# Optimization experiments

Measured on AMD Instinct MI355X. Metric: run time of the kernel, lower is better.

The kernel has to match this reference:

```python
import jax, jax.numpy as jnp
import numpy as np

VOCAB = 50257
EMB = 512
HID = 1024
H = HID // 2  # per-direction hidden
TAGS = 24
START = 22
STOP = 23
SEQ = 4096
NEG = -10000.0


def setup_inputs() -> dict:
    key = jax.random.key(0)
    ks = jax.random.split(key, 16)
    s = 1.0 / np.sqrt(H)
    u = lambda k, shp: jax.random.uniform(k, shp, jnp.float32, -s, s)
    sentence = jax.random.randint(ks[0], (SEQ,), 0, VOCAB)
    emb = jax.random.normal(ks[1], (VOCAB, EMB), jnp.float32)
    w_ih_f = u(ks[2], (4 * H, EMB)); w_hh_f = u(ks[3], (4 * H, H))
    b_ih_f = u(ks[4], (4 * H,));    b_hh_f = u(ks[5], (4 * H,))
    w_ih_b = u(ks[6], (4 * H, EMB)); w_hh_b = u(ks[7], (4 * H, H))
    b_ih_b = u(ks[8], (4 * H,));    b_hh_b = u(ks[9], (4 * H,))
    w_tag = u(ks[10], (TAGS, HID)); b_tag = u(ks[11], (TAGS,))
    transitions = jax.random.normal(ks[12], (TAGS, TAGS), jnp.float32)
    transitions = transitions.at[START, :].set(NEG).at[:, STOP].set(NEG)
    h0 = jax.random.normal(ks[13], (2, H), jnp.float32)  # [dir, H]
    c0 = jax.random.normal(ks[14], (2, H), jnp.float32)
    return dict(sentence=sentence, emb=emb,
                w_ih_f=w_ih_f, w_hh_f=w_hh_f, b_ih_f=b_ih_f, b_hh_f=b_hh_f,
                w_ih_b=w_ih_b, w_hh_b=w_hh_b, b_ih_b=b_ih_b, b_hh_b=b_hh_b,
                w_tag=w_tag, b_tag=b_tag, transitions=transitions, h0=h0, c0=c0)


def _lstm_dir(x, w_ih, w_hh, b_ih, b_hh, h, c, reverse):
    # x: [T, EMB]; precompute input projections once
    xg = x @ w_ih.T + (b_ih + b_hh)  # [T, 4H]
    def step(carry, xt):
        h, c = carry
        g = xt + h @ w_hh.T
        i, f, gg, o = jnp.split(g, 4)
        i = jax.nn.sigmoid(i); f = jax.nn.sigmoid(f)
        gg = jnp.tanh(gg);     o = jax.nn.sigmoid(o)
        c = f * c + i * gg
        h = o * jnp.tanh(c)
        return (h, c), h
    _, hs = jax.lax.scan(step, (h, c), xg, reverse=reverse)
    return hs  # [T, H]


def reference(sentence, emb, w_ih_f, w_hh_f, b_ih_f, b_hh_f,
              w_ih_b, w_hh_b, b_ih_b, b_hh_b, w_tag, b_tag,
              transitions, h0, c0):
    x = emb[sentence]  # [T, EMB]
    hf = _lstm_dir(x, w_ih_f, w_hh_f, b_ih_f, b_hh_f, h0[0], c0[0], False)
    hb = _lstm_dir(x, w_ih_b, w_hh_b, b_ih_b, b_hh_b, h0[1], c0[1], True)
    lstm_out = jnp.concatenate([hf, hb], axis=-1)          # [T, HID]
    feats = lstm_out @ w_tag.T + b_tag                     # [T, TAGS]

    # Viterbi: max-plus recursion over tags, vectorized per timestep
    fv0 = jnp.full((TAGS,), NEG, jnp.float32).at[START].set(0.0)
    def vstep(fv, feat):
        scores = transitions + fv[None, :]                 # [next, prev]
        bp = jnp.argmax(scores, axis=1)
        return jnp.max(scores, axis=1) + feat, bp
    fv, bps = jax.lax.scan(vstep, fv0, feats)              # bps: [T, TAGS]

    terminal = fv + transitions[STOP]
    best = jnp.argmax(terminal)
    path_score = terminal[best]

    def btstep(tag, bp):
        prev = bp[tag]
        return prev, prev
    _, ys = jax.lax.scan(btstep, best, bps, reverse=True)  # ys[t] = tag at t-1; ys[0]==START
    best_path = jnp.concatenate([ys[1:], best[None]]).astype(jnp.int32)
    return path_score, best_path
```

## Files before the change

kernel.cpp:

```cpp
#include <hip/hip_runtime.h>
#include <cstdint>
#include <cstddef>

#define T_SEQ 4096
#define EMB_D 512
#define HDIM 512
#define G4 2048
#define NTAGS 24
#define START_TAG 22
#define STOP_TAG 23
#define NEGV -10000.0f
#define NBLK 32
#define HSLICE 16
#define SENT 0xFFFFFFFFu

__global__ __launch_bounds__(256) void gemm_xg_kernel(
    const int* __restrict__ sent, const float* __restrict__ emb,
    const float* __restrict__ w_ih_f, const float* __restrict__ b_ih_f, const float* __restrict__ b_hh_f,
    const float* __restrict__ w_ih_b, const float* __restrict__ b_ih_b, const float* __restrict__ b_hh_b,
    float* __restrict__ xg)
{
    const int dir = blockIdx.z;
    const float* W  = dir ? w_ih_b : w_ih_f;
    const float* bi = dir ? b_ih_b : b_ih_f;
    const float* bh = dir ? b_hh_b : b_hh_f;
    const int m0 = blockIdx.y * 64;
    const int n0 = blockIdx.x * 64;
    const int tid = threadIdx.x;

    __shared__ __attribute__((aligned(16))) float As[32][64];
    __shared__ __attribute__((aligned(16))) float Bs[32][64];

    const int lrow = tid >> 2;
    const int lk   = (tid & 3) * 8;

    const int srow = sent[m0 + lrow];
    const float* aptr = emb + (size_t)srow * EMB_D + lk;
    const float* bptr = W   + (size_t)(n0 + lrow) * EMB_D + lk;

    const int ty = tid >> 4;
    const int tx = tid & 15;

    float acc[4][4];
    #pragma unroll
    for (int i = 0; i < 4; ++i)
        #pragma unroll
        for (int j = 0; j < 4; ++j) acc[i][j] = 0.f;

    for (int kk = 0; kk < EMB_D; kk += 32) {
        float4 a0 = *(const float4*)(aptr + kk);
        float4 a1 = *(const float4*)(aptr + kk + 4);
        float4 b0 = *(const float4*)(bptr + kk);
        float4 b1 = *(const float4*)(bptr + kk + 4);
        __syncthreads();
        As[lk+0][lrow]=a0.x; As[lk+1][lrow]=a0.y; As[lk+2][lrow]=a0.z; As[lk+3][lrow]=a0.w;
        As[lk+4][lrow]=a1.x; As[lk+5][lrow]=a1.y; As[lk+6][lrow]=a1.z; As[lk+7][lrow]=a1.w;
        Bs[lk+0][lrow]=b0.x; Bs[lk+1][lrow]=b0.y; Bs[lk+2][lrow]=b0.z; Bs[lk+3][lrow]=b0.w;
        Bs[lk+4][lrow]=b1.x; Bs[lk+5][lrow]=b1.y; Bs[lk+6][lrow]=b1.z; Bs[lk+7][lrow]=b1.w;
        __syncthreads();
        #pragma unroll
        for (int k = 0; k < 32; ++k) {
            float4 av = *(const float4*)&As[k][ty*4];
            float4 bv = *(const float4*)&Bs[k][tx*4];
            acc[0][0]+=av.x*bv.x; acc[0][1]+=av.x*bv.y; acc[0][2]+=av.x*bv.z; acc[0][3]+=av.x*bv.w;
            acc[1][0]+=av.y*bv.x; acc[1][1]+=av.y*bv.y; acc[1][2]+=av.y*bv.z; acc[1][3]+=av.y*bv.w;
            acc[2][0]+=av.z*bv.x; acc[2][1]+=av.z*bv.y; acc[2][2]+=av.z*bv.z; acc[2][3]+=av.z*bv.w;
            acc[3][0]+=av.w*bv.x; acc[3][1]+=av.w*bv.y; acc[3][2]+=av.w*bv.z; acc[3][3]+=av.w*bv.w;
        }
    }
    #pragma unroll
    for (int i = 0; i < 4; ++i) {
        const int t = m0 + ty*4 + i;
        float* crow = xg + ((size_t)dir*T_SEQ + t) * G4 + n0 + tx*4;
        #pragma unroll
        for (int j = 0; j < 4; ++j) {
            const int jg = n0 + tx*4 + j;
            crow[j] = acc[i][j] + bi[jg] + bh[jg];
        }
    }
}

__global__ __attribute__((amdgpu_waves_per_eu(2, 2))) __launch_bounds__(512)
void bilstm_kernel(
    const float* __restrict__ w_hh_f, const float* __restrict__ w_hh_b,
    const float* __restrict__ h0, const float* __restrict__ c0,
    const float* __restrict__ xg,
    uint32_t* __restrict__ h_hist,
    int* __restrict__ claim)
{
    uint32_t xcc;
    asm volatile("s_getreg_b32 %0, hwreg(HW_REG_XCC_ID)" : "=s"(xcc));
    xcc &= 7u;

    __shared__ int rank_s;
    if (threadIdx.x == 0)
        rank_s = __hip_atomic_fetch_add(&claim[xcc], 1, __ATOMIC_RELAXED,
                                        __HIP_MEMORY_SCOPE_AGENT);
    __syncthreads();
    const int rank = rank_s;

    int dir;
    if (xcc == 0) dir = 0;
    else if (xcc == 1) dir = 1;
    else return;
    if (rank >= NBLK) return;
    const int b = rank;

    const int tid = threadIdx.x;
    const int q   = tid >> 6;
    const int rl  = tid & 63;
    const int g2  = rl >> 4;
    const int hu  = rl & 15;
    const int row = g2 * HDIM + b * HSLICE + hu;

    const float* Wrow = (dir ? w_hh_b : w_hh_f) + (size_t)row * HDIM + q * 64;
    float w[64];
    #pragma unroll
    for (int j = 0; j < 16; ++j) {
        float4 v = ((const float4*)Wrow)[j];
        w[4*j+0]=v.x; w[4*j+1]=v.y; w[4*j+2]=v.z; w[4*j+3]=v.w;
    }
    #pragma unroll
    for (int i = 0; i < 64; ++i) asm volatile("" : "+v"(w[i]));

    __shared__ __attribute__((aligned(16))) float part[2][512];

    float c = (tid < HSLICE) ? c0[dir*HDIM + b*HSLICE + tid] : 0.f;

    const float* xgd = xg + (size_t)dir * T_SEQ * G4;
    uint32_t* hh = h_hist + (size_t)dir * T_SEQ * HDIM;

    float xv_cur = 0.f;
    if (tid < 64) {
        const int t0 = dir ? (T_SEQ - 1) : 0;
        xv_cur = xgd[(size_t)t0 * G4 + row];
    }

    for (int idx = 0; idx < T_SEQ; ++idx) {
        const int t = dir ? (T_SEQ - 1 - idx) : idx;

        float xv_nxt = 0.f;
        if (tid < 64 && idx + 1 < T_SEQ) {
            const int tn = dir ? (t - 1) : (t + 1);
            xv_nxt = xgd[(size_t)tn * G4 + row];
        }

        float hv;
        if (idx == 0) {
            hv = h0[dir*HDIM + tid];
        } else {
            const int tprev = dir ? (t + 1) : (t - 1);
            const uint32_t* wp = hh + (size_t)tprev*HDIM + tid;
            uint32_t u;
            do {
                u = __hip_atomic_load(wp, __ATOMIC_RELAXED, __HIP_MEMORY_SCOPE_AGENT);
            } while (u == SENT);
            union { uint32_t uu; float f; } cv; cv.uu = u;
            hv = cv.f;
        }

        const uint32_t hvu = __float_as_uint(hv);
        float s = 0.f;
        #pragma unroll
        for (int j = 0; j < 16; ++j) {
            const float h0v = __uint_as_float((uint32_t)__builtin_amdgcn_readlane((int)hvu, 4*j+0));
            const float h1v = __uint_as_float((uint32_t)__builtin_amdgcn_readlane((int)hvu, 4*j+1));
            const float h2v = __uint_as_float((uint32_t)__builtin_amdgcn_readlane((int)hvu, 4*j+2));
            const float h3v = __uint_as_float((uint32_t)__builtin_amdgcn_readlane((int)hvu, 4*j+3));
            s += w[4*j+0]*h0v + w[4*j+1]*h1v + w[4*j+2]*h2v + w[4*j+3]*h3v;
        }
        part[idx & 1][tid] = s;
        __syncthreads();

        if (tid < 64) {
            float g = xv_cur;
            const float* pb = part[idx & 1];
            #pragma unroll
            for (int qq = 0; qq < 8; ++qq) g += pb[qq*64 + tid];
            g = (g2 == 2) ? tanhf(g) : 1.f/(1.f + expf(-g));
            float iv = __shfl(g, hu);
            float fg = __shfl(g, hu + 16);
            float gv = __shfl(g, hu + 32);
            float ov = __shfl(g, hu + 48);
            if (tid < HSLICE) {
                c = fg*c + iv*gv;
                union { float f; uint32_t u; } hb; hb.f = ov * tanhf(c);
                __hip_atomic_store(hh + (size_t)t*HDIM + b*HSLICE + tid, hb.u,
                                   __ATOMIC_RELAXED, __HIP_MEMORY_SCOPE_AGENT);
            }
        }
        xv_cur = xv_nxt;
    }
}

__global__ __launch_bounds__(256) void feats_kernel(
    const float* __restrict__ h_hist, const float* __restrict__ w_tag,
    const float* __restrict__ b_tag, float* __restrict__ feats)
{
    const int t = blockIdx.x;
    const int tid = threadIdx.x;
    __shared__ __attribute__((aligned(16))) float h[1024];
    __shared__ float partl[192];
    for (int i = tid; i < 512; i += 256) {
        h[i]     = h_hist[(size_t)t*HDIM + i];
        h[512+i] = h_hist[(size_t)T_SEQ*HDIM + (size_t)t*HDIM + i];
    }
    __syncthreads();
    if (tid < 192) {
        const int tag = tid >> 3, p = tid & 7;
        const float* wr = w_tag + (size_t)tag*1024 + p*128;
        const float* hp = h + p*128;
        float s = 0.f;
        #pragma unroll 8
        for (int j = 0; j < 128; ++j) s += wr[j]*hp[j];
        partl[tid] = s;
    }
    __syncthreads();
    if (tid < NTAGS) {
        float s = b_tag[tid];
        #pragma unroll
        for (int p = 0; p < 8; ++p) s += partl[tid*8+p];
        feats[(size_t)t*NTAGS + tid] = s;
    }
}

__global__ void viterbi_fwd_kernel(
    const float* __restrict__ feats, const float* __restrict__ trans,
    float* __restrict__ d_out, unsigned char* __restrict__ bp,
    int* __restrict__ best_tag)
{
    const int lane = threadIdx.x;
    const bool act = lane < NTAGS;
    float tr[NTAGS];
    #pragma unroll
    for (int p = 0; p < NTAGS; ++p)
        tr[p] = act ? trans[lane*NTAGS + p] : NEGV;

    float fv = (lane == START_TAG) ? 0.f : NEGV;
    __shared__ float fvs[NTAGS];
    __shared__ float term[NTAGS];

    float ftn = act ? feats[lane] : 0.f;
    for (int t = 0; t < T_SEQ; ++t) {
        if (act) fvs[lane] = fv;
        __syncthreads();
        float ft = ftn;
        if (act && t + 1 < T_SEQ) ftn = feats[(size_t)(t+1)*NTAGS + lane];
        float bestv = -3.4e38f;
        int argp = 0;
        #pragma unroll
        for (int p = 0; p < NTAGS; ++p) {
            float sc = tr[p] + fvs[p];
            if (sc > bestv) { bestv = sc; argp = p; }
        }
        __syncthreads();
        fv = bestv + ft;
        if (act) bp[(size_t)t*NTAGS + lane] = (unsigned char)argp;
    }
    if (act) { fv += trans[STOP_TAG*NTAGS + lane]; term[lane] = fv; }
    __syncthreads();
    if (lane == 0) {
        float bv = term[0]; int bi = 0;
        #pragma unroll
        for (int p = 1; p < NTAGS; ++p) if (term[p] > bv) { bv = term[p]; bi = p; }
        d_out[0] = bv;
        *best_tag = bi;
    }
}

__global__ void bt_compose_kernel(const unsigned char* __restrict__ bp,
                                  unsigned char* __restrict__ segmap)
{
    const int s = blockIdx.x;
    const int tid = threadIdx.x;
    __shared__ __attribute__((aligned(16))) unsigned char lbp[64*NTAGS];
    const uint32_t* src = (const uint32_t*)(bp + (size_t)s * 64 * NTAGS);
    uint32_t* dst = (uint32_t*)lbp;
    #pragma unroll
    for (int i = 0; i < 6; ++i) dst[tid + 64*i] = src[tid + 64*i];
    __syncthreads();
    if (tid < NTAGS) {
        int m = tid;
        for (int tt = 63; tt >= 0; --tt) m = lbp[tt*NTAGS + m];
        segmap[s*NTAGS + tid] = (unsigned char)m;
    }
}

__global__ void bt_final_kernel(const unsigned char* __restrict__ segmap,
                                const int* __restrict__ best_tag,
                                int* __restrict__ end_tags)
{
    if (threadIdx.x == 0) {
        int tag = *best_tag;
        end_tags[63] = tag;
        for (int s = 63; s >= 1; --s) {
            tag = segmap[s*NTAGS + tag];
            end_tags[s-1] = tag;
        }
    }
}

__global__ void bt_write_kernel(const unsigned char* __restrict__ bp,
                                const int* __restrict__ end_tags,
                                float* __restrict__ out_path)
{
    const int s = blockIdx.x;
    const int tid = threadIdx.x;
    __shared__ __attribute__((aligned(16))) unsigned char lbp[64*NTAGS];
    const uint32_t* src = (const uint32_t*)(bp + (size_t)s * 64 * NTAGS);
    uint32_t* dst = (uint32_t*)lbp;
    #pragma unroll
    for (int i = 0; i < 6; ++i) dst[tid + 64*i] = src[tid + 64*i];
    __syncthreads();
    if (tid == 0) {
        int tag = end_tags[s];
        out_path[s*64 + 63] = (float)tag;
        for (int tt = 63; tt >= 1; --tt) {
            tag = lbp[tt*NTAGS + tag];
            out_path[s*64 + tt - 1] = (float)tag;
        }
    }
}

extern "C" void kernel_launch(void* const* d_in, const int* in_sizes, int n_in,
                              void* d_out, int out_size, void* d_ws, size_t ws_size,
                              hipStream_t stream)
{
    const int*   sent   = (const int*)d_in[0];
    const float* emb    = (const float*)d_in[1];
    const float* w_ih_f = (const float*)d_in[2];
    const float* w_hh_f = (const float*)d_in[3];
    const float* b_ih_f = (const float*)d_in[4];
    const float* b_hh_f = (const float*)d_in[5];
    const float* w_ih_b = (const float*)d_in[6];
    const float* w_hh_b = (const float*)d_in[7];
    const float* b_ih_b = (const float*)d_in[8];
    const float* b_hh_b = (const float*)d_in[9];
    const float* w_tag  = (const float*)d_in[10];
    const float* b_tag  = (const float*)d_in[11];
    const float* trans  = (const float*)d_in[12];
    const float* h0     = (const float*)d_in[13];
    const float* c0     = (const float*)d_in[14];
    float* out = (float*)d_out;

    char* ws = (char*)d_ws;
    size_t off = 0;
    auto alloc = [&](size_t bytes) {
        char* p = ws + off; off += (bytes + 255) & ~(size_t)255; return p;
    };
    float* xg      = (float*)alloc((size_t)2*T_SEQ*G4*sizeof(float));
    uint32_t* h_hist = (uint32_t*)alloc((size_t)2*T_SEQ*HDIM*sizeof(float));
    float* feats   = (float*)alloc((size_t)T_SEQ*NTAGS*sizeof(float));
    unsigned char* bp     = (unsigned char*)alloc((size_t)T_SEQ*NTAGS);
    unsigned char* segmap = (unsigned char*)alloc(64*NTAGS);
    int* best_tag = (int*)alloc(sizeof(int));
    int* end_tags = (int*)alloc(64*sizeof(int));
    int* claim    = (int*)alloc(8*sizeof(int));

    if (off > ws_size) {
        hipMemsetAsync(d_out, 0xFF, 4, stream);
        return;
    }

    hipMemsetAsync(h_hist, 0xFF, (size_t)2*T_SEQ*HDIM*sizeof(float), stream);
    hipMemsetAsync(claim, 0, 8*sizeof(int), stream);

    dim3 gg(G4/64, T_SEQ/64, 2);
    gemm_xg_kernel<<<gg, 256, 0, stream>>>(sent, emb,
        w_ih_f, b_ih_f, b_hh_f, w_ih_b, b_ih_b, b_hh_b, xg);
    bilstm_kernel<<<512, 512, 0, stream>>>(w_hh_f, w_hh_b, h0, c0, xg, h_hist, claim);
    feats_kernel<<<T_SEQ, 256, 0, stream>>>((const float*)h_hist, w_tag, b_tag, feats);
    viterbi_fwd_kernel<<<1, 64, 0, stream>>>(feats, trans, out, bp, best_tag);
    bt_compose_kernel<<<64, 64, 0, stream>>>(bp, segmap);
    bt_final_kernel<<<1, 64, 0, stream>>>(segmap, best_tag, end_tags);
    bt_write_kernel<<<64, 64, 0, stream>>>(bp, end_tags, out + 1);
}
```

Before: 8.850 ms.

## Restructure LSTM recurrent step so each wave owns whole hidden units

Work in the recurrent kernel is redistributed. Each wave now computes all four gates for two hidden units, with eight lanes splitting the K dimension. The incoming h vector is staged in padded LDS and read as float4, replacing 64 readlanes per lane. Partial sums are reduced with intra-wave shuffles, which removes the cross-wave LDS reduction, its second barrier, and the serial activation tail that ran only in wave 0. The cost is extra shuffle work and an LDS round trip for h on every timestep.

```diff
diff --git a/kernel.cpp b/kernel.cpp
--- a/kernel.cpp
+++ b/kernel.cpp
@@ -108,12 +108,14 @@
 
     const int tid = threadIdx.x;
     const int q   = tid >> 6;
-    const int rl  = tid & 63;
-    const int g2  = rl >> 4;
-    const int hu  = rl & 15;
-    const int row = g2 * HDIM + b * HSLICE + hu;
-
-    const float* Wrow = (dir ? w_hh_b : w_hh_f) + (size_t)row * HDIM + q * 64;
+    const int l   = tid & 63;
+    const int r   = l >> 3;
+    const int i   = l & 7;
+    const int gate = r & 3;
+    const int huo  = r >> 2;
+    const int row  = gate * HDIM + b * HSLICE + 2*q + huo;
+
+    const float* Wrow = (dir ? w_hh_b : w_hh_f) + (size_t)row * HDIM + i * 64;
     float w[64];
     #pragma unroll
     for (int j = 0; j < 16; ++j) {
@@ -121,29 +123,27 @@
         w[4*j+0]=v.x; w[4*j+1]=v.y; w[4*j+2]=v.z; w[4*j+3]=v.w;
     }
     #pragma unroll
-    for (int i = 0; i < 64; ++i) asm volatile("" : "+v"(w[i]));
-
-    __shared__ __attribute__((aligned(16))) float part[2][512];
-
-    float c = (tid < HSLICE) ? c0[dir*HDIM + b*HSLICE + tid] : 0.f;
+    for (int ii = 0; ii < 64; ++ii) asm volatile("" : "+v"(w[ii]));
+
+    __shared__ __attribute__((aligned(16))) float hbuf[2][544];
+
+    float c = 0.f;
+    if (i == 0 && gate == 0)
+        c = c0[dir*HDIM + b*HSLICE + 2*q + huo];
 
     const float* xgd = xg + (size_t)dir * T_SEQ * G4;
     uint32_t* hh = h_hist + (size_t)dir * T_SEQ * HDIM;
+    const bool leader = (i == 0);
 
     float xv_cur = 0.f;
-    if (tid < 64) {
+    if (leader) {
         const int t0 = dir ? (T_SEQ - 1) : 0;
         xv_cur = xgd[(size_t)t0 * G4 + row];
     }
 
     for (int idx = 0; idx < T_SEQ; ++idx) {
         const int t = dir ? (T_SEQ - 1 - idx) : idx;
-
-        float xv_nxt = 0.f;
-        if (tid < 64 && idx + 1 < T_SEQ) {
-            const int tn = dir ? (t - 1) : (t + 1);
-            xv_nxt = xgd[(size_t)tn * G4 + row];
-        }
+        const int p = idx & 1;
 
         float hv;
         if (idx == 0) {
@@ -158,36 +158,44 @@
             union { uint32_t uu; float f; } cv; cv.uu = u;
             hv = cv.f;
         }
-
-        const uint32_t hvu = __float_as_uint(hv);
+        hbuf[p][q*68 + l] = hv;
+        __syncthreads();
+
+        float xv_nxt = 0.f;
+        if (leader && idx + 1 < T_SEQ) {
+            const int tn = dir ? (t - 1) : (t + 1);
+            xv_nxt = xgd[(size_t)tn * G4 + row];
+        }
+
+        const float4* hb4 = (const float4*)&hbuf[p][i*68];
         float s = 0.f;
         #pragma unroll
         for (int j = 0; j < 16; ++j) {
-            const float h0v = __uint_as_float((uint32_t)__builtin_amdgcn_readlane((int)hvu, 4*j+0));
-            const float h1v = __uint_as_float((uint32_t)__builtin_amdgcn_readlane((int)hvu, 4*j+1));
-            const float h2v = __uint_as_float((uint32_t)__builtin_amdgcn_readlane((int)hvu, 4*j+2));
-            const float h3v = __uint_as_float((uint32_t)__builtin_amdgcn_readlane((int)hvu, 4*j+3));
-            s += w[4*j+0]*h0v + w[4*j+1]*h1v + w[4*j+2]*h2v + w[4*j+3]*h3v;
-        }
-        part[idx & 1][tid] = s;
-        __syncthreads();
-
-        if (tid < 64) {
-            float g = xv_cur;
-            const float* pb = part[idx & 1];
-            #pragma unroll
-            for (int qq = 0; qq < 8; ++qq) g += pb[qq*64 + tid];
-            g = (g2 == 2) ? tanhf(g) : 1.f/(1.f + expf(-g));
-            float iv = __shfl(g, hu);
-            float fg = __shfl(g, hu + 16);
-            float gv = __shfl(g, hu + 32);
-            float ov = __shfl(g, hu + 48);
-            if (tid < HSLICE) {
-                c = fg*c + iv*gv;
-                union { float f; uint32_t u; } hb; hb.f = ov * tanhf(c);
-                __hip_atomic_store(hh + (size_t)t*HDIM + b*HSLICE + tid, hb.u,
-                                   __ATOMIC_RELAXED, __HIP_MEMORY_SCOPE_AGENT);
-            }
+            float4 hvv = hb4[j];
+            s += w[4*j+0]*hvv.x + w[4*j+1]*hvv.y + w[4*j+2]*hvv.z + w[4*j+3]*hvv.w;
+        }
+
+        const int gbase = l & ~7;
+        float g = xv_cur + s;
+        #pragma unroll
+        for (int j = 1; j < 8; ++j) {
+            float pj = __shfl(s, gbase + j);
+            g += pj;
+        }
+
+        float act = (gate == 2) ? tanhf(g) : 1.f/(1.f + expf(-g));
+
+        const int base = l & 32;
+        float iv = __shfl(act, base + 0);
+        float fg = __shfl(act, base + 8);
+        float gv = __shfl(act, base + 16);
+        float ov = __shfl(act, base + 24);
+
+        if ((l & 31) == 0) {
+            c = fg*c + iv*gv;
+            union { float f; uint32_t u; } hb; hb.f = ov * tanhf(c);
+            __hip_atomic_store(hh + (size_t)t*HDIM + b*HSLICE + 2*q + (l>>5), hb.u,
+                               __ATOMIC_RELAXED, __HIP_MEMORY_SCOPE_AGENT);
         }
         xv_cur = xv_nxt;
     }
```

After: 8.296 ms. 1.07x faster.
